# Kernel tuning notes

Hardware: AMD Instinct MI355X
Metric: run time of the kernel (lower is better)

Reference implementation:

```python
import jax, jax.numpy as jnp
import numpy as np

N, CH, K, B = 30000, 96, 81, 8
HIDDEN = max(CH // 4, 8)
EPS = 1e-5


def setup_inputs() -> dict:
    key = jax.random.key(0)
    ks = jax.random.split(key, 12)
    feats = jax.random.normal(ks[0], (N, CH), dtype=jnp.float32)
    nbr_idx = jax.random.randint(ks[1], (N, K), 0, N).astype(jnp.int32)
    batch_ids = jnp.sort(jax.random.randint(ks[2], (N,), 0, B)).astype(jnp.int32)
    s = 1.0 / np.sqrt(CH * 1.0)
    W1 = jax.random.normal(ks[3], (K, CH, CH), dtype=jnp.float32) * s
    W2 = jax.random.normal(ks[4], (K, CH, CH), dtype=jnp.float32) * s
    g1 = jnp.ones((CH,), jnp.float32); b1 = jnp.zeros((CH,), jnp.float32)
    g2 = jnp.ones((CH,), jnp.float32); b2 = jnp.zeros((CH,), jnp.float32)
    fc1_w = jax.random.normal(ks[5], (CH, HIDDEN), dtype=jnp.float32) * s
    fc1_b = jnp.zeros((HIDDEN,), jnp.float32)
    fc2_w = jax.random.normal(ks[6], (HIDDEN, CH), dtype=jnp.float32) * (1.0 / np.sqrt(HIDDEN * 1.0))
    fc2_b = jnp.zeros((CH,), jnp.float32)
    return {"feats": feats, "W1": W1, "g1": g1, "b1": b1, "W2": W2,
            "g2": g2, "b2": b2, "fc1_w": fc1_w, "fc1_b": fc1_b,
            "fc2_w": fc2_w, "fc2_b": fc2_b, "nbr_idx": nbr_idx,
            "batch_ids": batch_ids}


def _sparse_conv(x, W, nbr):
    # gather-matmul-scatter form of MinkowskiConvolution (kernel map shared):
    # g: [N, K, ch] gathered neighbor features; contract each offset's [ch,ch] weight.
    g = x[nbr]
    return jnp.einsum('nkc,kcd->nd', g, W)


def _bn(x, gamma, beta):
    mu = jnp.mean(x, axis=0)
    var = jnp.var(x, axis=0)
    return gamma * (x - mu) * jax.lax.rsqrt(var + EPS) + beta


def _se(x, batch_ids, fc1_w, fc1_b, fc2_w, fc2_b):
    # MinkowskiGlobalAvgPooling: per-sample mean over points
    sums = jax.ops.segment_sum(x, batch_ids, num_segments=B)
    cnts = jax.ops.segment_sum(jnp.ones((x.shape[0], 1), x.dtype), batch_ids, num_segments=B)
    pooled = sums / jnp.maximum(cnts, 1.0)  # [B, ch]
    w = jax.nn.relu(pooled @ fc1_w + fc1_b)
    w = jax.nn.sigmoid(w @ fc2_w + fc2_b)   # [B, ch]
    return x * w[batch_ids]                  # broadcast multiplication


def reference(feats, W1, g1, b1, W2, g2, b2, fc1_w, fc1_b, fc2_w, fc2_b,
              nbr_idx, batch_ids):
    out = jax.nn.relu(_bn(_sparse_conv(feats, W1, nbr_idx), g1, b1))
    out = _bn(_sparse_conv(out, W2, nbr_idx), g2, b2)
    out = _se(out, batch_ids, fc1_w, fc1_b, fc2_w, fc2_b)
    return jax.nn.relu(out + feats)
```

## Files before the change

kernel.cpp:

```cpp
#include <hip/hip_runtime.h>
#include <hip/hip_bf16.h>

#define NPTS 30000
#define CH 96
#define KOFF 81
#define NB 8
#define HID 24
#define EPSV 1e-5f
#define RT 3
#define GSPLIT 625
#define KSPLIT 4

typedef __attribute__((ext_vector_type(8))) short bf16x8;
typedef __attribute__((ext_vector_type(4))) float f32x4;

__device__ __forceinline__ ushort f2bf(float f) {
    union { float f; unsigned int u; } x; x.f = f;
    unsigned int u = x.u;
    unsigned int r = (u + 0x7fffu + ((u >> 16) & 1u)) >> 16;
    return (ushort)r;
}

__device__ __forceinline__ void bn_coeffs(const float* __restrict__ ssum,
                                          const float* __restrict__ ssq,
                                          const float* __restrict__ g,
                                          const float* __restrict__ b,
                                          float* s_scale, float* s_shift) {
    int t = threadIdx.x;
    if (t < 96) {
        float mean = ssum[t] * (1.0f / NPTS);
        float var = ssq[t] * (1.0f / NPTS) - mean * mean;
        float sc = g[t] * rsqrtf(var + EPSV);
        s_scale[t] = sc;
        s_shift[t] = b[t] - mean * sc;
    }
    __syncthreads();
}

__global__ __launch_bounds__(256) void k_prep(const float* __restrict__ feats,
                                              const float* __restrict__ W1,
                                              const float* __restrict__ W2,
                                              const int* __restrict__ nbr,
                                              ushort* __restrict__ featsbf,
                                              float* __restrict__ outbuf,
                                              int* __restrict__ nbrT,
                                              ushort* __restrict__ wt1,
                                              ushort* __restrict__ wt2) {
    __shared__ __align__(16) char smem[36864];
    int bid = blockIdx.x, tid = threadIdx.x;
    if (bid < 2813) {
        int t = bid * 256 + tid;
        if (t < 720000) {
            float4 v = reinterpret_cast<const float4*>(feats)[t];
            ushort4 o;
            o.x = f2bf(v.x); o.y = f2bf(v.y); o.z = f2bf(v.z); o.w = f2bf(v.w);
            reinterpret_cast<ushort4*>(featsbf)[t] = o;
            float4 z = {0.f, 0.f, 0.f, 0.f};
            reinterpret_cast<float4*>(outbuf)[t] = z;
        }
    } else if (bid < 3282) {
        int* lds = (int*)smem;
        int n0 = (bid - 2813) * 64;
        int rows = min(64, NPTS - n0);
        int cnt = rows * 81;
        for (int i = tid; i < cnt; i += 256) lds[i] = nbr[n0 * 81 + i];
        __syncthreads();
        for (int o = tid; o < cnt; o += 256) {
            int kk = o / rows, r = o - kk * rows;
            nbrT[kk * NPTS + n0 + r] = lds[r * 81 + kk];
        }
    } else {
        float* lds = (float*)smem;
        int b = bid - 3282;
        int k = (b < 81) ? b : b - 81;
        const float* src = ((b < 81) ? W1 : W2) + k * 9216;
        ushort* dst = ((b < 81) ? wt1 : wt2) + k * 9216;
        for (int j = tid; j < 9216; j += 256) lds[j] = src[j];
        __syncthreads();
        for (int o = tid; o < 9216; o += 256) {
            int q = o / 768, rem = o - q * 768, d = rem >> 3, j = rem & 7;
            dst[o] = f2bf(lds[(q * 8 + j) * 96 + d]);
        }
    }
}

__global__ __launch_bounds__(64) void k_conv(const ushort* __restrict__ xbf,
                                             const ushort* __restrict__ wt,
                                             const int* __restrict__ nbrT,
                                             float* __restrict__ out) {
    const int lane = threadIdx.x;
    const int slice = blockIdx.x / GSPLIT;
    const int g = blockIdx.x % GSPLIT;
    const int k0 = slice * 20;
    const int k1 = k0 + ((slice == 3) ? 21 : 20);
    const int r16 = lane & 15, kg = lane >> 4;
    const int row0 = g * 48;

    f32x4 zero4 = {0.f, 0.f, 0.f, 0.f};
    f32x4 acc[RT][6];
#pragma unroll
    for (int rt = 0; rt < RT; ++rt)
#pragma unroll
        for (int db = 0; db < 6; ++db) acc[rt][db] = zero4;

    int idx[RT];
#pragma unroll
    for (int rt = 0; rt < RT; ++rt) idx[rt] = nbrT[k0 * NPTS + row0 + rt * 16 + r16];

    for (int k = k0; k < k1; ++k) {
        bf16x8 afrag[RT][3];
#pragma unroll
        for (int rt = 0; rt < RT; ++rt) {
            const ushort* as = xbf + idx[rt] * 96 + kg * 8;
#pragma unroll
            for (int c = 0; c < 3; ++c)
                afrag[rt][c] = *reinterpret_cast<const bf16x8*>(as + c * 32);
        }
        if (k + 1 < k1) {
#pragma unroll
            for (int rt = 0; rt < RT; ++rt)
                idx[rt] = nbrT[(k + 1) * NPTS + row0 + rt * 16 + r16];
        }
        const ushort* wk = wt + k * 9216;
#pragma unroll
        for (int c = 0; c < 3; ++c) {
            const int q = c * 4 + kg;
            bf16x8 bfrag[6];
#pragma unroll
            for (int db = 0; db < 6; ++db)
                bfrag[db] = *reinterpret_cast<const bf16x8*>(
                    wk + q * 768 + (db * 16 + r16) * 8);
#pragma unroll
            for (int rt = 0; rt < RT; ++rt)
#pragma unroll
                for (int db = 0; db < 6; ++db)
                    acc[rt][db] = __builtin_amdgcn_mfma_f32_16x16x32_bf16(
                        afrag[rt][c], bfrag[db], acc[rt][db], 0, 0, 0);
        }
    }

#pragma unroll
    for (int rt = 0; rt < RT; ++rt) {
        int rbase = row0 + rt * 16 + kg * 4;
#pragma unroll
        for (int db = 0; db < 6; ++db) {
            int col = db * 16 + r16;
#pragma unroll
            for (int i = 0; i < 4; ++i)
                atomicAdd(&out[(rbase + i) * 96 + col], acc[rt][db][i]);
        }
    }
}

__device__ __forceinline__ int lowb(const int* __restrict__ bids, int v) {
    int lo = 0, hi = NPTS;
    while (lo < hi) { int m = (lo + hi) >> 1; if (bids[m] < v) lo = m + 1; else hi = m; }
    return lo;
}

template <bool SEG>
__global__ __launch_bounds__(256) void k_stats(const float* __restrict__ y,
                                               const int* __restrict__ bids,
                                               float* __restrict__ ssum,
                                               float* __restrict__ ssq,
                                               float* __restrict__ segsum,
                                               float* __restrict__ cntf) {
    __shared__ float ls[96], lq[96], lg[96];
    int tid = threadIdx.x;
    if (tid < 96) { ls[tid] = 0.f; lq[tid] = 0.f; lg[tid] = 0.f; }
    __syncthreads();

    int b = 0, j, s, e;
    if (SEG) {
        b = blockIdx.x >> 5; j = blockIdx.x & 31;
        s = lowb(bids, b); e = lowb(bids, b + 1);
    } else {
        j = blockIdx.x; s = 0; e = NPTS;
    }
    const int stride = SEG ? (32 * 256) : (256 * 256);
    const int total = (e - s) * 24;
    const int base4 = s * 24;
    const int c40 = j * 256 + tid;

    f32x4 z = {0.f, 0.f, 0.f, 0.f};
    f32x4 sm[3] = {z, z, z}, sq[3] = {z, z, z};
    for (int c4 = c40; c4 < total; c4 += 3 * stride) {
#pragma unroll
        for (int m = 0; m < 3; ++m) {
            int c = c4 + m * stride;
            if (c < total) {
                f32x4 v = reinterpret_cast<const f32x4*>(y)[base4 + c];
                sm[m] += v; sq[m] += v * v;
            }
        }
    }
#pragma unroll
    for (int m = 0; m < 3; ++m) {
        int d0 = ((c40 + m * stride) * 4) % 96;
#pragma unroll
        for (int w = 0; w < 4; ++w) {
            atomicAdd(&ls[d0 + w], sm[m][w]);
            atomicAdd(&lq[d0 + w], sq[m][w]);
            if (SEG) atomicAdd(&lg[d0 + w], sm[m][w]);
        }
    }
    __syncthreads();
    if (tid < 96) {
        atomicAdd(&ssum[tid], ls[tid]);
        atomicAdd(&ssq[tid], lq[tid]);
        if (SEG) atomicAdd(&segsum[b * 96 + tid], lg[tid]);
    }
    if (SEG && tid == 0 && (blockIdx.x & 31) == 0) cntf[b] = (float)(e - s);
}

__global__ void k_apply1(float* __restrict__ x,
                         const float* __restrict__ ssum, const float* __restrict__ ssq,
                         const float* __restrict__ g, const float* __restrict__ b,
                         ushort* __restrict__ h) {
    __shared__ float scale[96], shift[96];
    bn_coeffs(ssum, ssq, g, b, scale, shift);
    int t = blockIdx.x * 256 + threadIdx.x;
    if (t >= 720000) return;
    float4 v = reinterpret_cast<const float4*>(x)[t];
    int d0 = (t * 4) % 96;
    ushort4 o;
    o.x = f2bf(fmaxf(v.x * scale[d0] + shift[d0], 0.f));
    o.y = f2bf(fmaxf(v.y * scale[d0 + 1] + shift[d0 + 1], 0.f));
    o.z = f2bf(fmaxf(v.z * scale[d0 + 2] + shift[d0 + 2], 0.f));
    o.w = f2bf(fmaxf(v.w * scale[d0 + 3] + shift[d0 + 3], 0.f));
    reinterpret_cast<ushort4*>(h)[t] = o;
    float4 z = {0.f, 0.f, 0.f, 0.f};
    reinterpret_cast<float4*>(x)[t] = z;
}

__global__ void k_se(const float* __restrict__ segsum, const float* __restrict__ cnt,
                     const float* __restrict__ ssum, const float* __restrict__ ssq,
                     const float* __restrict__ g, const float* __restrict__ b,
                     const float* __restrict__ fc1w, const float* __restrict__ fc1b,
                     const float* __restrict__ fc2w, const float* __restrict__ fc2b,
                     float* __restrict__ sew) {
    __shared__ float scale[96], shift[96];
    __shared__ float pooled[NB][96];
    __shared__ float hid[NB][HID];
    bn_coeffs(ssum, ssq, g, b, scale, shift);
    int t = threadIdx.x;
    for (int i = t; i < NB * 96; i += 256) {
        int bb = i / 96, d = i - bb * 96;
        pooled[bb][d] = segsum[i] / fmaxf(cnt[bb], 1.f) * scale[d] + shift[d];
    }
    __syncthreads();
    if (t < NB * HID) {
        int bb = t / HID, h = t - bb * HID;
        float s = fc1b[h];
        for (int d = 0; d < 96; ++d) s += pooled[bb][d] * fc1w[d * HID + h];
        hid[bb][h] = fmaxf(s, 0.f);
    }
    __syncthreads();
    for (int i = t; i < NB * 96; i += 256) {
        int bb = i / 96, d = i - bb * 96;
        float s = fc2b[d];
        for (int h = 0; h < HID; ++h) s += hid[bb][h] * fc2w[h * 96 + d];
        sew[i] = 1.f / (1.f + expf(-s));
    }
}

__global__ void k_final(const float* __restrict__ out2, const float* __restrict__ feats,
                        const float* __restrict__ ssum, const float* __restrict__ ssq,
                        const float* __restrict__ g, const float* __restrict__ b,
                        const float* __restrict__ sew, const int* __restrict__ bids,
                        float* __restrict__ out) {
    __shared__ float scale[96], shift[96];
    bn_coeffs(ssum, ssq, g, b, scale, shift);
    int t = blockIdx.x * 256 + threadIdx.x;
    if (t >= 720000) return;
    int e0 = t * 4;
    int n = e0 / 96;
    int d0 = e0 - n * 96;
    int bb = bids[n];
    const float* w = sew + bb * 96;
    float4 v = reinterpret_cast<const float4*>(out2)[t];
    float4 f = reinterpret_cast<const float4*>(feats)[t];
    float4 o;
    o.x = fmaxf((v.x * scale[d0] + shift[d0]) * w[d0] + f.x, 0.f);
    o.y = fmaxf((v.y * scale[d0 + 1] + shift[d0 + 1]) * w[d0 + 1] + f.y, 0.f);
    o.z = fmaxf((v.z * scale[d0 + 2] + shift[d0 + 2]) * w[d0 + 2] + f.z, 0.f);
    o.w = fmaxf((v.w * scale[d0 + 3] + shift[d0 + 3]) * w[d0 + 3] + f.w, 0.f);
    reinterpret_cast<float4*>(out)[t] = o;
}


extern "C" void kernel_launch(void* const* d_in, const int* in_sizes, int n_in,
                              void* d_out, int out_size, void* d_ws, size_t ws_size,
                              hipStream_t stream) {
    const float* feats = (const float*)d_in[0];
    const float* W1 = (const float*)d_in[1];
    const float* g1 = (const float*)d_in[2];
    const float* b1 = (const float*)d_in[3];
    const float* W2 = (const float*)d_in[4];
    const float* g2 = (const float*)d_in[5];
    const float* b2 = (const float*)d_in[6];
    const float* fc1w = (const float*)d_in[7];
    const float* fc1b = (const float*)d_in[8];
    const float* fc2w = (const float*)d_in[9];
    const float* fc2b = (const float*)d_in[10];
    const int* nbr = (const int*)d_in[11];
    const int* bids = (const int*)d_in[12];
    float* out = (float*)d_out;

    char* ws = (char*)d_ws;
    ushort* featsbf = (ushort*)(ws + 0);
    ushort* wt1 = (ushort*)(ws + 5760000);
    ushort* wt2 = (ushort*)(ws + 7252992);
    int* nbrT = (int*)(ws + 8745984);
    float* outbuf = (float*)(ws + 18465984);
    ushort* h1bf = (ushort*)(ws + 29985984);
    float* small = (float*)(ws + 35745984);
    float* sum1 = small + 0;
    float* sq1 = small + 96;
    float* sum2 = small + 192;
    float* sq2 = small + 288;
    float* segsum = small + 768;
    float* cntf = small + 1536;
    float* sew = small + 1544;

    const int gE = 2813;
    const int gC = KSPLIT * GSPLIT;

    hipMemsetAsync(small, 0, 16384, stream);
    k_prep<<<3444, 256, 0, stream>>>(feats, W1, W2, nbr, featsbf, outbuf, nbrT, wt1, wt2);

    k_conv<<<gC, 64, 0, stream>>>(featsbf, wt1, nbrT, outbuf);
    k_stats<false><<<256, 256, 0, stream>>>(outbuf, bids, sum1, sq1, segsum, cntf);
    k_apply1<<<gE, 256, 0, stream>>>(outbuf, sum1, sq1, g1, b1, h1bf);

    k_conv<<<gC, 64, 0, stream>>>(h1bf, wt2, nbrT, outbuf);
    k_stats<true><<<256, 256, 0, stream>>>(outbuf, bids, sum2, sq2, segsum, cntf);

    k_se<<<1, 256, 0, stream>>>(segsum, cntf, sum2, sq2, g2, b2, fc1w, fc1b, fc2w, fc2b, sew);
    k_final<<<gE, 256, 0, stream>>>(outbuf, feats, sum2, sq2, g2, b2, sew, bids, out);
}
```

Before: 364.6 us.

## Replace conv atomics with per-slice bf16 partials reduced in channel-major stats pass

```diff
diff --git a/kernel.cpp b/kernel.cpp
--- a/kernel.cpp
+++ b/kernel.cpp
@@ -10,6 +10,7 @@
 #define RT 3
 #define GSPLIT 625
 #define KSPLIT 4
+#define PSTRIDE (96 * NPTS)
 
 typedef __attribute__((ext_vector_type(8))) short bf16x8;
 typedef __attribute__((ext_vector_type(4))) float f32x4;
@@ -19,6 +20,9 @@
     unsigned int u = x.u;
     unsigned int r = (u + 0x7fffu + ((u >> 16) & 1u)) >> 16;
     return (ushort)r;
+}
+__device__ __forceinline__ float bf2f(ushort u) {
+    union { float f; unsigned int i; } x; x.i = ((unsigned int)u) << 16; return x.f;
 }
 
 __device__ __forceinline__ void bn_coeffs(const float* __restrict__ ssum,
@@ -37,15 +41,22 @@
     __syncthreads();
 }
 
+__device__ __forceinline__ int lowb(const int* __restrict__ bids, int v) {
+    int lo = 0, hi = NPTS;
+    while (lo < hi) { int m = (lo + hi) >> 1; if (bids[m] < v) lo = m + 1; else hi = m; }
+    return lo;
+}
+
 __global__ __launch_bounds__(256) void k_prep(const float* __restrict__ feats,
                                               const float* __restrict__ W1,
                                               const float* __restrict__ W2,
                                               const int* __restrict__ nbr,
+                                              const int* __restrict__ bids,
                                               ushort* __restrict__ featsbf,
-                                              float* __restrict__ outbuf,
                                               int* __restrict__ nbrT,
                                               ushort* __restrict__ wt1,
-                                              ushort* __restrict__ wt2) {
+                                              ushort* __restrict__ wt2,
+                                              int* __restrict__ boundsI) {
     __shared__ __align__(16) char smem[36864];
     int bid = blockIdx.x, tid = threadIdx.x;
     if (bid < 2813) {
@@ -55,8 +66,6 @@
             ushort4 o;
             o.x = f2bf(v.x); o.y = f2bf(v.y); o.z = f2bf(v.z); o.w = f2bf(v.w);
             reinterpret_cast<ushort4*>(featsbf)[t] = o;
-            float4 z = {0.f, 0.f, 0.f, 0.f};
-            reinterpret_cast<float4*>(outbuf)[t] = z;
         }
     } else if (bid < 3282) {
         int* lds = (int*)smem;
@@ -69,7 +78,7 @@
             int kk = o / rows, r = o - kk * rows;
             nbrT[kk * NPTS + n0 + r] = lds[r * 81 + kk];
         }
-    } else {
+    } else if (bid < 3444) {
         float* lds = (float*)smem;
         int b = bid - 3282;
         int k = (b < 81) ? b : b - 81;
@@ -81,13 +90,15 @@
             int q = o / 768, rem = o - q * 768, d = rem >> 3, j = rem & 7;
             dst[o] = f2bf(lds[(q * 8 + j) * 96 + d]);
         }
+    } else {
+        if (tid < 9) boundsI[tid] = lowb(bids, tid);
     }
 }
 
 __global__ __launch_bounds__(64) void k_conv(const ushort* __restrict__ xbf,
                                              const ushort* __restrict__ wt,
                                              const int* __restrict__ nbrT,
-                                             float* __restrict__ out) {
+                                             ushort* __restrict__ P) {
     const int lane = threadIdx.x;
     const int slice = blockIdx.x / GSPLIT;
     const int g = blockIdx.x % GSPLIT;
@@ -103,137 +114,222 @@
 #pragma unroll
         for (int db = 0; db < 6; ++db) acc[rt][db] = zero4;
 
-    int idx[RT];
-#pragma unroll
-    for (int rt = 0; rt < RT; ++rt) idx[rt] = nbrT[k0 * NPTS + row0 + rt * 16 + r16];
-
-    for (int k = k0; k < k1; ++k) {
-        bf16x8 afrag[RT][3];
-#pragma unroll
-        for (int rt = 0; rt < RT; ++rt) {
-            const ushort* as = xbf + idx[rt] * 96 + kg * 8;
+    int ia[RT], ib[RT];
+    bf16x8 aP[RT][3], aQ[RT][3];
+
+#pragma unroll
+    for (int rt = 0; rt < RT; ++rt) ia[rt] = nbrT[k0 * NPTS + row0 + rt * 16 + r16];
+#pragma unroll
+    for (int rt = 0; rt < RT; ++rt) {
+        const ushort* as = xbf + ia[rt] * 96 + kg * 8;
+#pragma unroll
+        for (int c = 0; c < 3; ++c) aP[rt][c] = *reinterpret_cast<const bf16x8*>(as + c * 32);
+    }
+    {
+        int kn = (k0 + 1 < k1) ? (k0 + 1) : k0;
+#pragma unroll
+        for (int rt = 0; rt < RT; ++rt) ib[rt] = nbrT[kn * NPTS + row0 + rt * 16 + r16];
+    }
+
+    int k = k0;
+    while (true) {
+        {
+            const ushort* wk = wt + k * 9216;
+            bf16x8 bfrag[3][6];
+#pragma unroll
+            for (int c = 0; c < 3; ++c) {
+                const int q = c * 4 + kg;
+#pragma unroll
+                for (int db = 0; db < 6; ++db)
+                    bfrag[c][db] = *reinterpret_cast<const bf16x8*>(
+                        wk + q * 768 + (db * 16 + r16) * 8);
+            }
+            if (k + 1 < k1) {
+#pragma unroll
+                for (int rt = 0; rt < RT; ++rt) {
+                    const ushort* as = xbf + ib[rt] * 96 + kg * 8;
+#pragma unroll
+                    for (int c = 0; c < 3; ++c)
+                        aQ[rt][c] = *reinterpret_cast<const bf16x8*>(as + c * 32);
+                }
+            }
+            if (k + 2 < k1) {
+#pragma unroll
+                for (int rt = 0; rt < RT; ++rt)
+                    ia[rt] = nbrT[(k + 2) * NPTS + row0 + rt * 16 + r16];
+            }
 #pragma unroll
             for (int c = 0; c < 3; ++c)
-                afrag[rt][c] = *reinterpret_cast<const bf16x8*>(as + c * 32);
-        }
-        if (k + 1 < k1) {
-#pragma unroll
-            for (int rt = 0; rt < RT; ++rt)
-                idx[rt] = nbrT[(k + 1) * NPTS + row0 + rt * 16 + r16];
-        }
-        const ushort* wk = wt + k * 9216;
-#pragma unroll
-        for (int c = 0; c < 3; ++c) {
-            const int q = c * 4 + kg;
-            bf16x8 bfrag[6];
-#pragma unroll
-            for (int db = 0; db < 6; ++db)
-                bfrag[db] = *reinterpret_cast<const bf16x8*>(
-                    wk + q * 768 + (db * 16 + r16) * 8);
-#pragma unroll
-            for (int rt = 0; rt < RT; ++rt)
+#pragma unroll
+                for (int rt = 0; rt < RT; ++rt)
+#pragma unroll
+                    for (int db = 0; db < 6; ++db)
+                        acc[rt][db] = __builtin_amdgcn_mfma_f32_16x16x32_bf16(
+                            aP[rt][c], bfrag[c][db], acc[rt][db], 0, 0, 0);
+        }
+        ++k; if (k >= k1) break;
+        {
+            const ushort* wk = wt + k * 9216;
+            bf16x8 bfrag[3][6];
+#pragma unroll
+            for (int c = 0; c < 3; ++c) {
+                const int q = c * 4 + kg;
 #pragma unroll
                 for (int db = 0; db < 6; ++db)
-                    acc[rt][db] = __builtin_amdgcn_mfma_f32_16x16x32_bf16(
-                        afrag[rt][c], bfrag[db], acc[rt][db], 0, 0, 0);
-        }
-    }
-
+                    bfrag[c][db] = *reinterpret_cast<const bf16x8*>(
+                        wk + q * 768 + (db * 16 + r16) * 8);
+            }
+            if (k + 1 < k1) {
+#pragma unroll
+                for (int rt = 0; rt < RT; ++rt) {
+                    const ushort* as = xbf + ia[rt] * 96 + kg * 8;
+#pragma unroll
+                    for (int c = 0; c < 3; ++c)
+                        aP[rt][c] = *reinterpret_cast<const bf16x8*>(as + c * 32);
+                }
+            }
+            if (k + 2 < k1) {
+#pragma unroll
+                for (int rt = 0; rt < RT; ++rt)
+                    ib[rt] = nbrT[(k + 2) * NPTS + row0 + rt * 16 + r16];
+            }
+#pragma unroll
+            for (int c = 0; c < 3; ++c)
+#pragma unroll
+                for (int rt = 0; rt < RT; ++rt)
+#pragma unroll
+                    for (int db = 0; db < 6; ++db)
+                        acc[rt][db] = __builtin_amdgcn_mfma_f32_16x16x32_bf16(
+                            aQ[rt][c], bfrag[c][db], acc[rt][db], 0, 0, 0);
+        }
+        ++k; if (k >= k1) break;
+    }
+
+    ushort* Ps = P + slice * PSTRIDE;
 #pragma unroll
     for (int rt = 0; rt < RT; ++rt) {
-        int rbase = row0 + rt * 16 + kg * 4;
+        int rowb = row0 + rt * 16 + kg * 4;
 #pragma unroll
         for (int db = 0; db < 6; ++db) {
             int col = db * 16 + r16;
-#pragma unroll
-            for (int i = 0; i < 4; ++i)
-                atomicAdd(&out[(rbase + i) * 96 + col], acc[rt][db][i]);
-        }
-    }
-}
-
-__device__ __forceinline__ int lowb(const int* __restrict__ bids, int v) {
-    int lo = 0, hi = NPTS;
-    while (lo < hi) { int m = (lo + hi) >> 1; if (bids[m] < v) lo = m + 1; else hi = m; }
-    return lo;
+            ushort4 o;
+            o.x = f2bf(acc[rt][db][0]); o.y = f2bf(acc[rt][db][1]);
+            o.z = f2bf(acc[rt][db][2]); o.w = f2bf(acc[rt][db][3]);
+            *reinterpret_cast<ushort4*>(Ps + col * NPTS + rowb) = o;
+        }
+    }
 }
 
 template <bool SEG>
-__global__ __launch_bounds__(256) void k_stats(const float* __restrict__ y,
-                                               const int* __restrict__ bids,
-                                               float* __restrict__ ssum,
-                                               float* __restrict__ ssq,
-                                               float* __restrict__ segsum,
-                                               float* __restrict__ cntf) {
-    __shared__ float ls[96], lq[96], lg[96];
+__global__ __launch_bounds__(256) void k_stats2(const ushort* __restrict__ P,
+                                                ushort* __restrict__ y,
+                                                float* __restrict__ ssum,
+                                                float* __restrict__ ssq,
+                                                float* __restrict__ segsum,
+                                                const int* __restrict__ boundsI) {
+    __shared__ int lb[9];
+    __shared__ float red[10][4];
+    const int col = blockIdx.x / 12;
+    const int chunk = blockIdx.x % 12;
+    const int tid = threadIdx.x;
+    if (tid < 9) lb[tid] = boundsI[tid];
+    __syncthreads();
+    const int nbase = chunk * 2500;
+    const int cb = col * NPTS;
+
+    float s = 0.f, sq = 0.f;
+    float seg[8] = {0.f, 0.f, 0.f, 0.f, 0.f, 0.f, 0.f, 0.f};
+    for (int r = tid * 4; r < 2500; r += 1024) {
+        int n = nbase + r;
+        float v0 = 0.f, v1 = 0.f, v2 = 0.f, v3 = 0.f;
+#pragma unroll
+        for (int sl = 0; sl < KSPLIT; ++sl) {
+            ushort4 u = *reinterpret_cast<const ushort4*>(P + sl * PSTRIDE + cb + n);
+            v0 += bf2f(u.x); v1 += bf2f(u.y); v2 += bf2f(u.z); v3 += bf2f(u.w);
+        }
+        ushort4 o; o.x = f2bf(v0); o.y = f2bf(v1); o.z = f2bf(v2); o.w = f2bf(v3);
+        *reinterpret_cast<ushort4*>(y + cb + n) = o;
+        s += v0 + v1 + v2 + v3;
+        sq += v0 * v0 + v1 * v1 + v2 * v2 + v3 * v3;
+        if (SEG) {
+            float vv[4] = {v0, v1, v2, v3};
+#pragma unroll
+            for (int j = 0; j < 4; ++j) {
+                int nj = n + j, bb = 0;
+#pragma unroll
+                for (int t = 1; t < 8; ++t) bb += (nj >= lb[t]) ? 1 : 0;
+#pragma unroll
+                for (int q = 0; q < 8; ++q) seg[q] += (bb == q) ? vv[j] : 0.f;
+            }
+        }
+    }
+#pragma unroll
+    for (int off = 32; off; off >>= 1) {
+        s += __shfl_xor(s, off); sq += __shfl_xor(sq, off);
+        if (SEG)
+#pragma unroll
+            for (int q = 0; q < 8; ++q) seg[q] += __shfl_xor(seg[q], off);
+    }
+    int wave = tid >> 6, lane = tid & 63;
+    if (lane == 0) {
+        red[0][wave] = s; red[1][wave] = sq;
+        if (SEG)
+#pragma unroll
+            for (int q = 0; q < 8; ++q) red[2 + q][wave] = seg[q];
+    }
+    __syncthreads();
+    int nred = SEG ? 10 : 2;
+    if (tid < nred) {
+        float v = red[tid][0] + red[tid][1] + red[tid][2] + red[tid][3];
+        if (tid == 0) atomicAdd(&ssum[col], v);
+        else if (tid == 1) atomicAdd(&ssq[col], v);
+        else atomicAdd(&segsum[(tid - 2) * 96 + col], v);
+    }
+}
+
+__global__ __launch_bounds__(256) void k_apply1(const ushort* __restrict__ y,
+                                                const float* __restrict__ ssum,
+                                                const float* __restrict__ ssq,
+                                                const float* __restrict__ g,
+                                                const float* __restrict__ b,
+                                                ushort* __restrict__ h1) {
+    __shared__ float scale[96], shift[96];
+    __shared__ ushort ybuf[96][72];
+    bn_coeffs(ssum, ssq, g, b, scale, shift);
     int tid = threadIdx.x;
-    if (tid < 96) { ls[tid] = 0.f; lq[tid] = 0.f; lg[tid] = 0.f; }
-    __syncthreads();
-
-    int b = 0, j, s, e;
-    if (SEG) {
-        b = blockIdx.x >> 5; j = blockIdx.x & 31;
-        s = lowb(bids, b); e = lowb(bids, b + 1);
-    } else {
-        j = blockIdx.x; s = 0; e = NPTS;
-    }
-    const int stride = SEG ? (32 * 256) : (256 * 256);
-    const int total = (e - s) * 24;
-    const int base4 = s * 24;
-    const int c40 = j * 256 + tid;
-
-    f32x4 z = {0.f, 0.f, 0.f, 0.f};
-    f32x4 sm[3] = {z, z, z}, sq[3] = {z, z, z};
-    for (int c4 = c40; c4 < total; c4 += 3 * stride) {
-#pragma unroll
-        for (int m = 0; m < 3; ++m) {
-            int c = c4 + m * stride;
-            if (c < total) {
-                f32x4 v = reinterpret_cast<const f32x4*>(y)[base4 + c];
-                sm[m] += v; sq[m] += v * v;
-            }
-        }
-    }
-#pragma unroll
-    for (int m = 0; m < 3; ++m) {
-        int d0 = ((c40 + m * stride) * 4) % 96;
-#pragma unroll
-        for (int w = 0; w < 4; ++w) {
-            atomicAdd(&ls[d0 + w], sm[m][w]);
-            atomicAdd(&lq[d0 + w], sq[m][w]);
-            if (SEG) atomicAdd(&lg[d0 + w], sm[m][w]);
-        }
-    }
-    __syncthreads();
-    if (tid < 96) {
-        atomicAdd(&ssum[tid], ls[tid]);
-        atomicAdd(&ssq[tid], lq[tid]);
-        if (SEG) atomicAdd(&segsum[b * 96 + tid], lg[tid]);
-    }
-    if (SEG && tid == 0 && (blockIdx.x & 31) == 0) cntf[b] = (float)(e - s);
-}
-
-__global__ void k_apply1(float* __restrict__ x,
-                         const float* __restrict__ ssum, const float* __restrict__ ssq,
-                         const float* __restrict__ g, const float* __restrict__ b,
-                         ushort* __restrict__ h) {
-    __shared__ float scale[96], shift[96];
-    bn_coeffs(ssum, ssq, g, b, scale, shift);
-    int t = blockIdx.x * 256 + threadIdx.x;
-    if (t >= 720000) return;
-    float4 v = reinterpret_cast<const float4*>(x)[t];
-    int d0 = (t * 4) % 96;
-    ushort4 o;
-    o.x = f2bf(fmaxf(v.x * scale[d0] + shift[d0], 0.f));
-    o.y = f2bf(fmaxf(v.y * scale[d0 + 1] + shift[d0 + 1], 0.f));
-    o.z = f2bf(fmaxf(v.z * scale[d0 + 2] + shift[d0 + 2], 0.f));
-    o.w = f2bf(fmaxf(v.w * scale[d0 + 3] + shift[d0 + 3], 0.f));
-    reinterpret_cast<ushort4*>(h)[t] = o;
-    float4 z = {0.f, 0.f, 0.f, 0.f};
-    reinterpret_cast<float4*>(x)[t] = z;
-}
-
-__global__ void k_se(const float* __restrict__ segsum, const float* __restrict__ cnt,
+    int n0 = blockIdx.x * 64;
+    int rows = min(64, NPTS - n0);
+    for (int it = tid; it < 96 * 16; it += 256) {
+        int col = it >> 4, rc = it & 15;
+        if (rc * 4 < rows) {
+            ushort4 u = *reinterpret_cast<const ushort4*>(y + col * NPTS + n0 + rc * 4);
+            float sc = scale[col], sh = shift[col];
+            ushort4 o;
+            o.x = f2bf(fmaxf(bf2f(u.x) * sc + sh, 0.f));
+            o.y = f2bf(fmaxf(bf2f(u.y) * sc + sh, 0.f));
+            o.z = f2bf(fmaxf(bf2f(u.z) * sc + sh, 0.f));
+            o.w = f2bf(fmaxf(bf2f(u.w) * sc + sh, 0.f));
+            *reinterpret_cast<ushort4*>(&ybuf[col][rc * 4]) = o;
+        }
+    }
+    __syncthreads();
+    int row = tid >> 2, cg = tid & 3;
+    if (row < rows) {
+        unsigned int w[12];
+#pragma unroll
+        for (int j = 0; j < 12; ++j) {
+            int c0 = cg * 24 + j * 2;
+            unsigned int lo = ybuf[c0][row], hi = ybuf[c0 + 1][row];
+            w[j] = lo | (hi << 16);
+        }
+        uint4* dst = reinterpret_cast<uint4*>(h1 + (n0 + row) * 96 + cg * 24);
+        dst[0] = make_uint4(w[0], w[1], w[2], w[3]);
+        dst[1] = make_uint4(w[4], w[5], w[6], w[7]);
+        dst[2] = make_uint4(w[8], w[9], w[10], w[11]);
+    }
+}
+
+__global__ void k_se(const float* __restrict__ segsum, const int* __restrict__ boundsI,
                      const float* __restrict__ ssum, const float* __restrict__ ssq,
                      const float* __restrict__ g, const float* __restrict__ b,
                      const float* __restrict__ fc1w, const float* __restrict__ fc1b,
@@ -246,7 +342,8 @@
     int t = threadIdx.x;
     for (int i = t; i < NB * 96; i += 256) {
         int bb = i / 96, d = i - bb * 96;
-        pooled[bb][d] = segsum[i] / fmaxf(cnt[bb], 1.f) * scale[d] + shift[d];
+        float cb = (float)(boundsI[bb + 1] - boundsI[bb]);
+        pooled[bb][d] = segsum[i] / fmaxf(cb, 1.f) * scale[d] + shift[d];
     }
     __syncthreads();
     if (t < NB * HID) {
@@ -264,28 +361,58 @@
     }
 }
 
-__global__ void k_final(const float* __restrict__ out2, const float* __restrict__ feats,
-                        const float* __restrict__ ssum, const float* __restrict__ ssq,
-                        const float* __restrict__ g, const float* __restrict__ b,
-                        const float* __restrict__ sew, const int* __restrict__ bids,
-                        float* __restrict__ out) {
+__global__ __launch_bounds__(256) void k_final(const ushort* __restrict__ y2,
+                                               const float* __restrict__ feats,
+                                               const float* __restrict__ ssum,
+                                               const float* __restrict__ ssq,
+                                               const float* __restrict__ g,
+                                               const float* __restrict__ b,
+                                               const float* __restrict__ sew,
+                                               const int* __restrict__ boundsI,
+                                               float* __restrict__ out) {
     __shared__ float scale[96], shift[96];
+    __shared__ float fbuf[96][68];
+    __shared__ float sewl[NB * 96];
+    __shared__ int lb[9];
     bn_coeffs(ssum, ssq, g, b, scale, shift);
-    int t = blockIdx.x * 256 + threadIdx.x;
-    if (t >= 720000) return;
-    int e0 = t * 4;
-    int n = e0 / 96;
-    int d0 = e0 - n * 96;
-    int bb = bids[n];
-    const float* w = sew + bb * 96;
-    float4 v = reinterpret_cast<const float4*>(out2)[t];
-    float4 f = reinterpret_cast<const float4*>(feats)[t];
-    float4 o;
-    o.x = fmaxf((v.x * scale[d0] + shift[d0]) * w[d0] + f.x, 0.f);
-    o.y = fmaxf((v.y * scale[d0 + 1] + shift[d0 + 1]) * w[d0 + 1] + f.y, 0.f);
-    o.z = fmaxf((v.z * scale[d0 + 2] + shift[d0 + 2]) * w[d0 + 2] + f.z, 0.f);
-    o.w = fmaxf((v.w * scale[d0 + 3] + shift[d0 + 3]) * w[d0 + 3] + f.w, 0.f);
-    reinterpret_cast<float4*>(out)[t] = o;
+    int tid = threadIdx.x;
+    for (int i = tid; i < NB * 96; i += 256) sewl[i] = sew[i];
+    if (tid < 9) lb[tid] = boundsI[tid];
+    int n0 = blockIdx.x * 64;
+    int rows = min(64, NPTS - n0);
+    for (int it = tid; it < 96 * 16; it += 256) {
+        int col = it >> 4, rc = it & 15;
+        if (rc * 4 < rows) {
+            ushort4 u = *reinterpret_cast<const ushort4*>(y2 + col * NPTS + n0 + rc * 4);
+            float sc = scale[col], sh = shift[col];
+            f32x4 v;
+            v[0] = bf2f(u.x) * sc + sh; v[1] = bf2f(u.y) * sc + sh;
+            v[2] = bf2f(u.z) * sc + sh; v[3] = bf2f(u.w) * sc + sh;
+            *reinterpret_cast<f32x4*>(&fbuf[col][rc * 4]) = v;
+        }
+    }
+    __syncthreads();
+    int row = tid >> 2, cg = tid & 3;
+    if (row < rows) {
+        int n = n0 + row;
+        int bb = 0;
+#pragma unroll
+        for (int t = 1; t < 8; ++t) bb += (n >= lb[t]) ? 1 : 0;
+        const float* swr = &sewl[bb * 96];
+        const float* fr = feats + n * 96 + cg * 24;
+        float* orow = out + n * 96 + cg * 24;
+#pragma unroll
+        for (int t4 = 0; t4 < 6; ++t4) {
+            float4 fv = *reinterpret_cast<const float4*>(fr + t4 * 4);
+            int c0 = cg * 24 + t4 * 4;
+            float4 o;
+            o.x = fmaxf(fbuf[c0 + 0][row] * swr[c0 + 0] + fv.x, 0.f);
+            o.y = fmaxf(fbuf[c0 + 1][row] * swr[c0 + 1] + fv.y, 0.f);
+            o.z = fmaxf(fbuf[c0 + 2][row] * swr[c0 + 2] + fv.z, 0.f);
+            o.w = fmaxf(fbuf[c0 + 3][row] * swr[c0 + 3] + fv.w, 0.f);
+            *reinterpret_cast<float4*>(orow + t4 * 4) = o;
+        }
+    }
 }
 
 
@@ -312,30 +439,32 @@
     ushort* wt1 = (ushort*)(ws + 5760000);
     ushort* wt2 = (ushort*)(ws + 7252992);
     int* nbrT = (int*)(ws + 8745984);
-    float* outbuf = (float*)(ws + 18465984);
-    ushort* h1bf = (ushort*)(ws + 29985984);
-    float* small = (float*)(ws + 35745984);
+    ushort* P = (ushort*)(ws + 18465984);
+    ushort* y = (ushort*)(ws + 41505984);
+    ushort* h1bf = (ushort*)(ws + 47265984);
+    float* small = (float*)(ws + 53025984);
     float* sum1 = small + 0;
     float* sq1 = small + 96;
     float* sum2 = small + 192;
     float* sq2 = small + 288;
-    float* segsum = small + 768;
-    float* cntf = small + 1536;
-    float* sew = small + 1544;
-
-    const int gE = 2813;
+    float* segsum = small + 384;
+    float* sew = small + 1152;
+    int* boundsI = (int*)(small + 1920);
+
     const int gC = KSPLIT * GSPLIT;
+    const int gS = 96 * 12;
+    const int gT = 469;
 
     hipMemsetAsync(small, 0, 16384, stream);
-    k_prep<<<3444, 256, 0, stream>>>(feats, W1, W2, nbr, featsbf, outbuf, nbrT, wt1, wt2);
-
-    k_conv<<<gC, 64, 0, stream>>>(featsbf, wt1, nbrT, outbuf);
-    k_stats<false><<<256, 256, 0, stream>>>(outbuf, bids, sum1, sq1, segsum, cntf);
-    k_apply1<<<gE, 256, 0, stream>>>(outbuf, sum1, sq1, g1, b1, h1bf);
-
-    k_conv<<<gC, 64, 0, stream>>>(h1bf, wt2, nbrT, outbuf);
-    k_stats<true><<<256, 256, 0, stream>>>(outbuf, bids, sum2, sq2, segsum, cntf);
-
-    k_se<<<1, 256, 0, stream>>>(segsum, cntf, sum2, sq2, g2, b2, fc1w, fc1b, fc2w, fc2b, sew);
-    k_final<<<gE, 256, 0, stream>>>(outbuf, feats, sum2, sq2, g2, b2, sew, bids, out);
-}
+    k_prep<<<3445, 256, 0, stream>>>(feats, W1, W2, nbr, bids, featsbf, nbrT, wt1, wt2, boundsI);
+
+    k_conv<<<gC, 64, 0, stream>>>(featsbf, wt1, nbrT, P);
+    k_stats2<false><<<gS, 256, 0, stream>>>(P, y, sum1, sq1, segsum, boundsI);
+    k_apply1<<<gT, 256, 0, stream>>>(y, sum1, sq1, g1, b1, h1bf);
+
+    k_conv<<<gC, 64, 0, stream>>>(h1bf, wt2, nbrT, P);
+    k_stats2<true><<<gS, 256, 0, stream>>>(P, y, sum2, sq2, segsum, boundsI);
+
+    k_se<<<1, 256, 0, stream>>>(segsum, boundsI, sum2, sq2, g2, b2, fc1w, fc1b, fc2w, fc2b, sew);
+    k_final<<<gT, 256, 0, stream>>>(y, feats, sum2, sq2, g2, b2, sew, boundsI, out);
+}
```

Measured after the change: 384.1 us. 1.05x slower.
